# Kernel optimization log

Measured on AMD Instinct MI355X. Metric: run time of the kernel, lower is better.

## Reference

```python
import jax, jax.numpy as jnp
import numpy as np

N_NODES = 100000
N_EDGES = 20000
N_INC = 800000


def hconv(node_idx, edge_idx, X, w, W, b):
    # node -> hyperedge: weighted mean of member node features
    msg = X[node_idx] * w[node_idx, None]                      # [I, d]
    e_sum = jax.ops.segment_sum(msg, edge_idx, num_segments=N_EDGES)
    e_den = jax.ops.segment_sum(w[node_idx], edge_idx, num_segments=N_EDGES)
    e_feat = e_sum / jnp.maximum(e_den, 1e-6)[:, None]         # [E, d]
    # hyperedge -> node: mean over incident hyperedges
    v_sum = jax.ops.segment_sum(e_feat[edge_idx], node_idx, num_segments=N_NODES)
    v_deg = jax.ops.segment_sum(jnp.ones((edge_idx.shape[0],), X.dtype),
                                node_idx, num_segments=N_NODES)
    v_feat = v_sum / jnp.maximum(v_deg, 1.0)[:, None]          # [N, d]
    return v_feat @ W + b


def setup_inputs() -> dict:
    key = jax.random.key(0)
    k1, k2, k3, k4, k5, k6 = jax.random.split(key, 6)
    d, h, c = 256, 16, 40
    H = jax.random.normal(k1, (N_NODES, d), dtype=jnp.float32)
    input_weight = jax.random.uniform(k2, (N_NODES,), dtype=jnp.float32)
    node_idx = jax.random.randint(k3, (N_INC,), 0, N_NODES, dtype=jnp.int32)
    edge_idx = jax.random.randint(k4, (N_INC,), 0, N_EDGES, dtype=jnp.int32)
    W1 = jax.random.normal(k5, (d, h), dtype=jnp.float32) / np.sqrt(d)
    b1 = jnp.zeros((h,), jnp.float32)
    W2 = jax.random.normal(k6, (h, c), dtype=jnp.float32) / np.sqrt(h)
    b2 = jnp.zeros((c,), jnp.float32)
    return {"H": H, "input_weight": input_weight, "node_idx": node_idx,
            "edge_idx": edge_idx, "W1": W1, "b1": b1, "W2": W2, "b2": b2}


def reference(H, input_weight, node_idx, edge_idx, W1, b1, W2, b2):
    x = jax.nn.relu(hconv(node_idx, edge_idx, H, input_weight, W1, b1))
    # dropout is identity at inference (training=False)
    x = hconv(node_idx, edge_idx, x, input_weight, W2, b2)
    return jax.nn.log_softmax(x, axis=1)
```

## Files before the change

kernel.cpp:

```cpp
#include <hip/hip_runtime.h>

#define N_NODES 100000
#define N_EDGES 20000
#define N_INC   800000
#define D_IN    256
#define D_H     16
#define D_OUT   40

#define EBS    32
#define NBE    625
#define ECAP   1600
#define VBS    256
#define NBV    392
#define VCAP   2400
#define TE     4096
#define EPART  196
#define TV     6144
#define NPART  131
#define PTOT   327
#define GEMM_BLOCKS 782
#define CPAD   16

typedef short bf16x8 __attribute__((ext_vector_type(8)));
typedef float f32x4  __attribute__((ext_vector_type(4)));

__device__ __forceinline__ unsigned short f2bf(float f) {
    unsigned u = __float_as_uint(f);
    unsigned r = u + 0x7FFF + ((u >> 16) & 1);
    return (unsigned short)(r >> 16);
}

__device__ __forceinline__ int block_exscan512(int local, int* sc8) {
    int t = threadIdx.x, lane = t & 63, wid = t >> 6;
    int s = local;
#pragma unroll
    for (int o = 1; o < 64; o <<= 1) {
        int x = __shfl_up(s, o, 64);
        if (lane >= o) s += x;
    }
    if (lane == 63) sc8[wid] = s;
    __syncthreads();
    int wbase = 0;
#pragma unroll
    for (int i = 0; i < 8; ++i) if (i < wid) wbase += sc8[i];
    return wbase + s - local;
}

__global__ __launch_bounds__(512) void init_kernel(
    const float* __restrict__ W1, unsigned short* __restrict__ bfrag,
    int* __restrict__ cnts ) {
    int t = threadIdx.x;
    for (int i = t; i < (NBE + NBV) * CPAD; i += 512) cnts[i] = 0;
    int c = t >> 6, l = t & 63;
    int n = l & 15, q = l >> 4;
    unsigned short v[8];
#pragma unroll
    for (int j = 0; j < 8; ++j)
        v[j] = f2bf(W1[(c * 32 + q * 8 + j) * D_H + n]);
    *(int4*)(bfrag + (size_t)(c * 64 + l) * 8) = *(int4*)v;
}

union SMemP {
    struct { int lrec[TE]; int lhist[NBE]; int lbase[NBE];
             int gbase[NBE]; int lcur[NBE]; int sc[8]; } pe;
    struct { int lrec[TV]; int lhist[NBV]; int lbase[NBV];
             int gbase[NBV]; int lcur[NBV]; int sc[8]; } pn;
};

__global__ __launch_bounds__(512) void part_kernel(
    const int* __restrict__ ni, const int* __restrict__ ei,
    int* __restrict__ cnt_be, int* __restrict__ cnt_bv,
    int* __restrict__ staged_e, int* __restrict__ staged_v) {
    __shared__ SMemP sm;
    int t = threadIdx.x;
    if (blockIdx.x < EPART) {
        int base = blockIdx.x * TE;
        int rec[TE / 512];
        for (int i = t; i < NBE; i += 512) sm.pe.lhist[i] = 0;
        __syncthreads();
#pragma unroll
        for (int r = 0; r < TE / 512; ++r) {
            int idx = base + r * 512 + t;
            rec[r] = -1;
            if (idx < N_INC) {
                int e = ei[idx], v = ni[idx];
                int key = e >> 5;
                rec[r] = v | ((e & 31) << 17) | (key << 22);
                atomicAdd(&sm.pe.lhist[key], 1);
            }
        }
        __syncthreads();
        int b0 = 2 * t, b1 = 2 * t + 1;
        int h0 = (b0 < NBE) ? sm.pe.lhist[b0] : 0;
        int h1 = (b1 < NBE) ? sm.pe.lhist[b1] : 0;
        int ex = block_exscan512(h0 + h1, sm.pe.sc);
        if (b0 < NBE) {
            sm.pe.lbase[b0] = ex; sm.pe.lcur[b0] = ex;
            sm.pe.gbase[b0] = h0 ? (b0 * ECAP + atomicAdd(&cnt_be[b0 * CPAD], h0)) : 0;
        }
        if (b1 < NBE) {
            int ex1 = ex + h0;
            sm.pe.lbase[b1] = ex1; sm.pe.lcur[b1] = ex1;
            sm.pe.gbase[b1] = h1 ? (b1 * ECAP + atomicAdd(&cnt_be[b1 * CPAD], h1)) : 0;
        }
        __syncthreads();
#pragma unroll
        for (int r = 0; r < TE / 512; ++r) {
            if (rec[r] != -1) {
                int key = ((unsigned)rec[r]) >> 22;
                int p = atomicAdd(&sm.pe.lcur[key], 1);
                sm.pe.lrec[p] = rec[r];
            }
        }
        __syncthreads();
        int total = min(TE, N_INC - base);
        for (int i = t; i < total; i += 512) {
            int rr = sm.pe.lrec[i];
            int bk = ((unsigned)rr) >> 22;
            int dst = sm.pe.gbase[bk] + (i - sm.pe.lbase[bk]);
            if (dst < (bk + 1) * ECAP) staged_e[dst] = rr;
        }
    } else {
        int base = (blockIdx.x - EPART) * TV;
        int rec[TV / 512];
        for (int i = t; i < NBV; i += 512) sm.pn.lhist[i] = 0;
        __syncthreads();
#pragma unroll
        for (int r = 0; r < TV / 512; ++r) {
            int idx = base + r * 512 + t;
            rec[r] = -1;
            if (idx < N_INC) {
                int e = ei[idx], v = ni[idx];
                int key = v >> 8;
                rec[r] = e | ((v & 255) << 15) | (key << 23);
                atomicAdd(&sm.pn.lhist[key], 1);
            }
        }
        __syncthreads();
        int h = (t < NBV) ? sm.pn.lhist[t] : 0;
        int ex = block_exscan512(h, sm.pn.sc);
        if (t < NBV) {
            sm.pn.lbase[t] = ex; sm.pn.lcur[t] = ex;
            sm.pn.gbase[t] = h ? (t * VCAP + atomicAdd(&cnt_bv[t * CPAD], h)) : 0;
        }
        __syncthreads();
#pragma unroll
        for (int r = 0; r < TV / 512; ++r) {
            if (rec[r] != -1) {
                int key = ((unsigned)rec[r]) >> 23;
                int p = atomicAdd(&sm.pn.lcur[key], 1);
                sm.pn.lrec[p] = rec[r];
            }
        }
        __syncthreads();
        int total = min(TV, N_INC - base);
        for (int i = t; i < total; i += 512) {
            int rr = sm.pn.lrec[i];
            int bk = ((unsigned)rr) >> 23;
            int dst = sm.pn.gbase[bk] + (i - sm.pn.lbase[bk]);
            if (dst < (bk + 1) * VCAP) staged_v[dst] = rr;
        }
    }
}

__global__ __launch_bounds__(512) void gemm_kernel(
    const float* __restrict__ H, const unsigned short* __restrict__ bfrag,
    const float* __restrict__ w, float* __restrict__ T) {
    int wave = (blockIdx.x * 512 + threadIdx.x) >> 6;
    if (wave >= N_NODES / 16) return;
    int lane = threadIdx.x & 63;
    int m = lane & 15, q = lane >> 4;
    int row0 = wave * 16;
    const float4* hp = (const float4*)(H + (size_t)(row0 + m) * D_IN) + q * 2;

    float4 la[16];
#pragma unroll
    for (int c = 0; c < 8; ++c) {
        la[2 * c]     = hp[c * 8];
        la[2 * c + 1] = hp[c * 8 + 1];
    }
    bf16x8 bf[8];
    const int4* bp = (const int4*)bfrag;
#pragma unroll
    for (int c = 0; c < 8; ++c) {
        int4 raw = bp[c * 64 + lane];
        bf[c] = *(bf16x8*)&raw;
    }
    f32x4 acc = {0.f, 0.f, 0.f, 0.f};
#pragma unroll
    for (int c = 0; c < 8; ++c) {
        float4 lo = la[2 * c], hi = la[2 * c + 1];
        bf16x8 af;
        af[0] = f2bf(lo.x); af[1] = f2bf(lo.y); af[2] = f2bf(lo.z); af[3] = f2bf(lo.w);
        af[4] = f2bf(hi.x); af[5] = f2bf(hi.y); af[6] = f2bf(hi.z); af[7] = f2bf(hi.w);
        acc = __builtin_amdgcn_mfma_f32_16x16x32_bf16(af, bf[c], acc, 0, 0, 0);
    }
#pragma unroll
    for (int r = 0; r < 4; ++r) {
        int row = row0 + q * 4 + r;
        T[(size_t)row * D_H + m] = acc[r] * w[row];
    }
}

union SMemS {
    struct { int lsort[ECAP]; int hist[EBS]; int cursor[EBS]; int lbeg[EBS]; } e;
    struct { int lsort[VCAP]; int hist[VBS]; int cursor[VBS]; int sc[8]; } v;
};

__global__ __launch_bounds__(512) void sortE_gA1_sortN_kernel(
    const int* __restrict__ cnt_be, int* __restrict__ staged_e,
    int2* __restrict__ off_e2,
    const int* __restrict__ cnt_bv, int* __restrict__ staged_v,
    int2* __restrict__ off_v2,
    const float* __restrict__ T, const float* __restrict__ w,
    float* __restrict__ e_den, float* __restrict__ e_feat) {
    __shared__ SMemS sm;
    int t = threadIdx.x;
    if (blockIdx.x < NBE) {
        int b = blockIdx.x;
        int beg = b * ECAP, cnt = min(cnt_be[b * CPAD], ECAP);
        if (t < EBS) sm.e.hist[t] = 0;
        __syncthreads();
        int rec[4], key[4], nr = 0;
#pragma unroll
        for (int r = 0; r < 4; ++r) {
            int k = r * 512 + t;
            if (k < cnt) {
                rec[nr] = staged_e[beg + k];
                key[nr] = (rec[nr] >> 17) & 31;
                atomicAdd(&sm.e.hist[key[nr]], 1);
                ++nr;
            }
        }
        __syncthreads();
        if (t < EBS) {
            int hh = sm.e.hist[t], s = hh;
#pragma unroll
            for (int o = 1; o < EBS; o <<= 1) {
                int x = __shfl_up(s, o, 64);
                if (t >= o) s += x;
            }
            int ex = s - hh;
            sm.e.cursor[t] = ex; sm.e.lbeg[t] = ex;
            off_e2[b * EBS + t] = make_int2(beg + ex, beg + ex + hh);
        }
        __syncthreads();
        for (int r = 0; r < nr; ++r) {
            int p = atomicAdd(&sm.e.cursor[key[r]], 1);
            sm.e.lsort[p] = rec[r];
        }
        __syncthreads();
        for (int i = t; i < cnt; i += 512) staged_e[beg + i] = sm.e.lsort[i];
        int el = t >> 4, j = t & 15;
        int lo = sm.e.lbeg[el], hi = lo + sm.e.hist[el];
        float acc = 0.f;
        int k = lo;
        for (; k + 4 <= hi; k += 4) {
            int r0 = sm.e.lsort[k]     & 0x1FFFF;
            int r1 = sm.e.lsort[k + 1] & 0x1FFFF;
            int r2 = sm.e.lsort[k + 2] & 0x1FFFF;
            int r3 = sm.e.lsort[k + 3] & 0x1FFFF;
            float t0 = T[(size_t)r0 * D_H + j];
            float t1 = T[(size_t)r1 * D_H + j];
            float t2 = T[(size_t)r2 * D_H + j];
            float t3 = T[(size_t)r3 * D_H + j];
            acc += t0; acc += t1; acc += t2; acc += t3;
        }
        for (; k < hi; ++k) acc += T[(size_t)(sm.e.lsort[k] & 0x1FFFF) * D_H + j];
        float den = 0.f;
        for (int k2 = lo + j; k2 < hi; k2 += 16) den += w[sm.e.lsort[k2] & 0x1FFFF];
#pragma unroll
        for (int o = 1; o < 16; o <<= 1) den += __shfl_xor(den, o, 64);
        int e = b * EBS + el;
        e_feat[(size_t)e * D_H + j] = acc / fmaxf(den, 1e-6f);
        if (j == 0) e_den[e] = den;
    } else {
        int b = blockIdx.x - NBE;
        int beg = b * VCAP, cnt = min(cnt_bv[b * CPAD], VCAP);
        for (int i = t; i < VBS; i += 512) sm.v.hist[i] = 0;
        __syncthreads();
        int rec[5], key[5], nr = 0;
#pragma unroll
        for (int r = 0; r < 5; ++r) {
            int k = r * 512 + t;
            if (k < cnt) {
                rec[nr] = staged_v[beg + k];
                key[nr] = (rec[nr] >> 15) & 255;
                atomicAdd(&sm.v.hist[key[nr]], 1);
                ++nr;
            }
        }
        __syncthreads();
        int hh = (t < VBS) ? sm.v.hist[t] : 0;
        int ex = block_exscan512(hh, sm.v.sc);
        if (t < VBS) {
            sm.v.cursor[t] = ex;
            int n = b * VBS + t;
            if (n < N_NODES) off_v2[n] = make_int2(beg + ex, beg + ex + hh);
        }
        __syncthreads();
        for (int r = 0; r < nr; ++r) {
            int p = atomicAdd(&sm.v.cursor[key[r]], 1);
            sm.v.lsort[p] = rec[r];
        }
        __syncthreads();
        for (int i = t; i < cnt; i += 512) staged_v[beg + i] = sm.v.lsort[i];
    }
}

__global__ __launch_bounds__(512) void gatherB1_kernel(
    const int2* __restrict__ off_v2, const int* __restrict__ staged_v,
    const float* __restrict__ e_feat, const float* __restrict__ w,
    const float* __restrict__ b1, float* __restrict__ out) {
    int t = blockIdx.x * 512 + threadIdx.x;
    int n = t >> 2;
    if (n >= N_NODES) return;
    int c = (t & 3) << 2;
    int2 be = off_v2[n];
    f32x4 acc = {0.f, 0.f, 0.f, 0.f};
    for (int k = be.x; k < be.y; ++k) {
        int e = staged_v[k] & 0x7FFF;
        acc += *(const f32x4*)(e_feat + (size_t)e * D_H + c);
    }
    float inv = 1.f / fmaxf((float)(be.y - be.x), 1.f);
    f32x4 bb = *(const f32x4*)(b1 + c);
    float wn = w[n];
    f32x4 r;
#pragma unroll
    for (int i = 0; i < 4; ++i) r[i] = fmaxf(acc[i] * inv + bb[i], 0.f) * wn;
    *(f32x4*)(out + (size_t)n * D_H + c) = r;
}

__global__ __launch_bounds__(512) void gatherA2_kernel(
    const int2* __restrict__ off_e2, const int* __restrict__ staged_e,
    const float* __restrict__ X, const float* __restrict__ e_den,
    float* __restrict__ e_feat) {
    int e = (blockIdx.x * 512 + threadIdx.x) >> 6;
    if (e >= N_EDGES) return;
    int lane = threadIdx.x & 63;
    int g = lane >> 2, c = (lane & 3) << 2;
    int2 be = off_e2[e];
    f32x4 acc = {0.f, 0.f, 0.f, 0.f};
    for (int k = be.x + g; k < be.y; k += 16) {
        int rec = staged_e[k];
        int v = rec & 0x1FFFF;
        acc += *(const f32x4*)(X + (size_t)v * D_H + c);
    }
#pragma unroll
    for (int s = 4; s <= 32; s <<= 1) {
        acc[0] += __shfl_xor(acc[0], s, 64);
        acc[1] += __shfl_xor(acc[1], s, 64);
        acc[2] += __shfl_xor(acc[2], s, 64);
        acc[3] += __shfl_xor(acc[3], s, 64);
    }
    if (lane < 4) {
        float inv = 1.f / fmaxf(e_den[e], 1e-6f);
        f32x4 r = acc * inv;
        *(f32x4*)(e_feat + (size_t)e * D_H + c) = r;
    }
}

__global__ __launch_bounds__(512) void gatherB2_final_kernel(
    const int2* __restrict__ off_v2, const int* __restrict__ staged_v,
    const float* __restrict__ e_feat,
    const float* __restrict__ W2, const float* __restrict__ b2,
    float* __restrict__ out) {
    __shared__ float sy[128 * 20];
    __shared__ float sW2[D_H * D_OUT];
    __shared__ float sb2[D_OUT];
    int t = threadIdx.x;
    for (int i = t; i < D_H * D_OUT; i += 512) sW2[i] = W2[i];
    if (t < D_OUT) sb2[t] = b2[t];
    int nl = t >> 2, c = (t & 3) << 2;
    int n = blockIdx.x * 128 + nl;
    f32x4 y = {0.f, 0.f, 0.f, 0.f};
    if (n < N_NODES) {
        int2 be = off_v2[n];
        f32x4 acc = {0.f, 0.f, 0.f, 0.f};
        for (int k = be.x; k < be.y; ++k) {
            int e = staged_v[k] & 0x7FFF;
            acc += *(const f32x4*)(e_feat + (size_t)e * D_H + c);
        }
        float inv = 1.f / fmaxf((float)(be.y - be.x), 1.f);
        y = acc * inv;
    }
    *(f32x4*)(sy + nl * 20 + c) = y;
    __syncthreads();
    if (n >= N_NODES) return;
    int c0 = (t & 3) * 10;
    float z[10];
#pragma unroll
    for (int i = 0; i < 10; ++i) z[i] = sb2[c0 + i];
#pragma unroll
    for (int jj = 0; jj < D_H; ++jj) {
        float yy = sy[nl * 20 + jj];
#pragma unroll
        for (int i = 0; i < 10; ++i) z[i] += yy * sW2[jj * D_OUT + c0 + i];
    }
    float m = z[0];
#pragma unroll
    for (int i = 1; i < 10; ++i) m = fmaxf(m, z[i]);
    m = fmaxf(m, __shfl_xor(m, 1, 64));
    m = fmaxf(m, __shfl_xor(m, 2, 64));
    float se = 0.f;
#pragma unroll
    for (int i = 0; i < 10; ++i) se += __expf(z[i] - m);
    se += __shfl_xor(se, 1, 64);
    se += __shfl_xor(se, 2, 64);
    float lse = m + __logf(se);
    float* op = out + (size_t)n * D_OUT + c0;
#pragma unroll
    for (int i = 0; i < 10; ++i) op[i] = z[i] - lse;
}

extern "C" void kernel_launch(void* const* d_in, const int* in_sizes, int n_in,
                              void* d_out, int out_size, void* d_ws, size_t ws_size,
                              hipStream_t stream) {
    const float* H  = (const float*)d_in[0];
    const float* w  = (const float*)d_in[1];
    const int*   ni = (const int*)d_in[2];
    const int*   ei = (const int*)d_in[3];
    const float* W1 = (const float*)d_in[4];
    const float* b1 = (const float*)d_in[5];
    const float* W2 = (const float*)d_in[6];
    const float* b2 = (const float*)d_in[7];
    float* out = (float*)d_out;

    int*            ws_i     = (int*)d_ws;
    int*            cnt_be   = ws_i + 0;
    int*            cnt_bv   = ws_i + 10000;
    unsigned short* bfrag    = (unsigned short*)(ws_i + 16272);
    int2*           off_e2   = (int2*)(ws_i + 18320);
    int2*           off_v2   = (int2*)(ws_i + 58320);
    int*            staged_e = ws_i + 258320;
    int*            staged_v = ws_i + 1258320;
    float*          e_den    = (float*)(ws_i + 2199120);
    float*          T        = (float*)(ws_i + 2219120);
    float*          e_feat   = (float*)(ws_i + 3819120);
    float*          x1       = (float*)(ws_i + 4139120);

    init_kernel<<<1, 512, 0, stream>>>(W1, bfrag, cnt_be);

    part_kernel<<<PTOT, 512, 0, stream>>>(ni, ei, cnt_be, cnt_bv,
                                          staged_e, staged_v);

    gemm_kernel<<<GEMM_BLOCKS, 512, 0, stream>>>(H, bfrag, w, T);

    sortE_gA1_sortN_kernel<<<NBE + NBV, 512, 0, stream>>>(
        cnt_be, staged_e, off_e2, cnt_bv, staged_v, off_v2, T, w, e_den, e_feat);

    gatherB1_kernel<<<782, 512, 0, stream>>>(off_v2, staged_v, e_feat, w, b1, x1);

    gatherA2_kernel<<<2500, 512, 0, stream>>>(off_e2, staged_e, x1, e_den, e_feat);

    gatherB2_final_kernel<<<782, 512, 0, stream>>>(
        off_v2, staged_v, e_feat, W2, b2, out);
}
```

Measured before the change: 252.6 us.

## Merge partition and GEMM kernels into one interleaved launch

Folds the incidence partitioning kernel and the bf16 MFMA GEMM kernel into a single launch. Block indices are interleaved three partition blocks to seven GEMM blocks, so the latency-bound atomic partitioning runs alongside the bandwidth-bound GEMM instead of one after the other, and one launch boundary is removed. The merged kernel also gets __launch_bounds__(512,2), and GEMM blocks now carry the partition kernel's large shared-memory union, which may reduce occupancy.

```diff
diff --git a/kernel.cpp b/kernel.cpp
--- a/kernel.cpp
+++ b/kernel.cpp
@@ -19,6 +19,7 @@
 #define NPART  131
 #define PTOT   327
 #define GEMM_BLOCKS 782
+#define GRID_K1 1120
 #define CPAD   16
 
 typedef short bf16x8 __attribute__((ext_vector_type(8)));
@@ -67,14 +68,58 @@
              int gbase[NBV]; int lcur[NBV]; int sc[8]; } pn;
 };
 
-__global__ __launch_bounds__(512) void part_kernel(
+__global__ __launch_bounds__(512, 2) void part_gemm_kernel(
     const int* __restrict__ ni, const int* __restrict__ ei,
+    const float* __restrict__ w,
     int* __restrict__ cnt_be, int* __restrict__ cnt_bv,
-    int* __restrict__ staged_e, int* __restrict__ staged_v) {
+    int* __restrict__ staged_e, int* __restrict__ staged_v,
+    const float* __restrict__ H, const unsigned short* __restrict__ bfrag,
+    float* __restrict__ T) {
     __shared__ SMemP sm;
     int t = threadIdx.x;
-    if (blockIdx.x < EPART) {
-        int base = blockIdx.x * TE;
+    int m10 = blockIdx.x % 10, g10 = blockIdx.x / 10;
+    bool is_part = (m10 < 3);
+    int pj = g10 * 3 + m10;
+    int gj = g10 * 7 + (m10 - 3);
+    if (is_part && pj >= PTOT) return;
+    if (!is_part && gj >= GEMM_BLOCKS) return;
+
+    if (!is_part) {
+        int wave = (gj * 512 + t) >> 6;
+        if (wave >= N_NODES / 16) return;
+        int lane = t & 63;
+        int m = lane & 15, q = lane >> 4;
+        int row0 = wave * 16;
+        const float4* hp = (const float4*)(H + (size_t)(row0 + m) * D_IN) + q * 2;
+        float4 la[16];
+#pragma unroll
+        for (int c = 0; c < 8; ++c) {
+            la[2 * c]     = hp[c * 8];
+            la[2 * c + 1] = hp[c * 8 + 1];
+        }
+        bf16x8 bf[8];
+        const int4* bp = (const int4*)bfrag;
+#pragma unroll
+        for (int c = 0; c < 8; ++c) {
+            int4 raw = bp[c * 64 + lane];
+            bf[c] = *(bf16x8*)&raw;
+        }
+        f32x4 acc = {0.f, 0.f, 0.f, 0.f};
+#pragma unroll
+        for (int c = 0; c < 8; ++c) {
+            float4 lo = la[2 * c], hi = la[2 * c + 1];
+            bf16x8 af;
+            af[0] = f2bf(lo.x); af[1] = f2bf(lo.y); af[2] = f2bf(lo.z); af[3] = f2bf(lo.w);
+            af[4] = f2bf(hi.x); af[5] = f2bf(hi.y); af[6] = f2bf(hi.z); af[7] = f2bf(hi.w);
+            acc = __builtin_amdgcn_mfma_f32_16x16x32_bf16(af, bf[c], acc, 0, 0, 0);
+        }
+#pragma unroll
+        for (int r = 0; r < 4; ++r) {
+            int row = row0 + q * 4 + r;
+            T[(size_t)row * D_H + m] = acc[r] * w[row];
+        }
+    } else if (pj < EPART) {
+        int base = pj * TE;
         int rec[TE / 512];
         for (int i = t; i < NBE; i += 512) sm.pe.lhist[i] = 0;
         __syncthreads();
@@ -121,7 +166,7 @@
             if (dst < (bk + 1) * ECAP) staged_e[dst] = rr;
         }
     } else {
-        int base = (blockIdx.x - EPART) * TV;
+        int base = (pj - EPART) * TV;
         int rec[TV / 512];
         for (int i = t; i < NBV; i += 512) sm.pn.lhist[i] = 0;
         __syncthreads();
@@ -160,45 +205,6 @@
             int dst = sm.pn.gbase[bk] + (i - sm.pn.lbase[bk]);
             if (dst < (bk + 1) * VCAP) staged_v[dst] = rr;
         }
-    }
-}
-
-__global__ __launch_bounds__(512) void gemm_kernel(
-    const float* __restrict__ H, const unsigned short* __restrict__ bfrag,
-    const float* __restrict__ w, float* __restrict__ T) {
-    int wave = (blockIdx.x * 512 + threadIdx.x) >> 6;
-    if (wave >= N_NODES / 16) return;
-    int lane = threadIdx.x & 63;
-    int m = lane & 15, q = lane >> 4;
-    int row0 = wave * 16;
-    const float4* hp = (const float4*)(H + (size_t)(row0 + m) * D_IN) + q * 2;
-
-    float4 la[16];
-#pragma unroll
-    for (int c = 0; c < 8; ++c) {
-        la[2 * c]     = hp[c * 8];
-        la[2 * c + 1] = hp[c * 8 + 1];
-    }
-    bf16x8 bf[8];
-    const int4* bp = (const int4*)bfrag;
-#pragma unroll
-    for (int c = 0; c < 8; ++c) {
-        int4 raw = bp[c * 64 + lane];
-        bf[c] = *(bf16x8*)&raw;
-    }
-    f32x4 acc = {0.f, 0.f, 0.f, 0.f};
-#pragma unroll
-    for (int c = 0; c < 8; ++c) {
-        float4 lo = la[2 * c], hi = la[2 * c + 1];
-        bf16x8 af;
-        af[0] = f2bf(lo.x); af[1] = f2bf(lo.y); af[2] = f2bf(lo.z); af[3] = f2bf(lo.w);
-        af[4] = f2bf(hi.x); af[5] = f2bf(hi.y); af[6] = f2bf(hi.z); af[7] = f2bf(hi.w);
-        acc = __builtin_amdgcn_mfma_f32_16x16x32_bf16(af, bf[c], acc, 0, 0, 0);
-    }
-#pragma unroll
-    for (int r = 0; r < 4; ++r) {
-        int row = row0 + q * 4 + r;
-        T[(size_t)row * D_H + m] = acc[r] * w[row];
     }
 }
 
@@ -441,10 +447,8 @@
 
     init_kernel<<<1, 512, 0, stream>>>(W1, bfrag, cnt_be);
 
-    part_kernel<<<PTOT, 512, 0, stream>>>(ni, ei, cnt_be, cnt_bv,
-                                          staged_e, staged_v);
-
-    gemm_kernel<<<GEMM_BLOCKS, 512, 0, stream>>>(H, bfrag, w, T);
+    part_gemm_kernel<<<GRID_K1, 512, 0, stream>>>(
+        ni, ei, w, cnt_be, cnt_bv, staged_e, staged_v, H, bfrag, T);
 
     sortE_gA1_sortN_kernel<<<NBE + NBV, 512, 0, stream>>>(
         cnt_be, staged_e, off_e2, cnt_bv, staged_v, off_v2, T, w, e_den, e_feat);
```

Result: faster. 242.0 us (-4.2%).
